# Optimization experiments

Measured on AMD Instinct MI355X. Metric: run time of the kernel, lower is better.

The kernel has to match this reference:

```python
import jax, jax.numpy as jnp
import numpy as np

B = 65536
N_PTS = 11        # n_trajectory_points
N_NEWTON = 5      # shooting_max_iter (fixed-count Newton shooting)
METRIC_FLOOR = 0.1


def _metric(c, lam, W1, b1, W2, b2, W3, b3):
    # g(c, lambda) > 0 ; c, lam: [B]
    x = jnp.stack([c, lam], axis=-1)              # [B, 2]
    h = jnp.tanh(x @ W1 + b1)
    h = jnp.tanh(h @ W2 + b2)
    return jax.nn.softplus((h @ W3 + b3)[..., 0]) + METRIC_FLOOR


def _christoffel(c, lam, mp):
    # 1-D manifold: Gamma = 0.5 * (dg/dc) / g  (dg/dc via forward-mode jvp)
    g, dg = jax.jvp(lambda cc: _metric(cc, lam, *mp), (c,), (jnp.ones_like(c),))
    return 0.5 * dg / g


def _integrate(c0, v0, lam, mp, n_pts):
    # RK4 integration of geodesic ODE  c' = v, v' = -Gamma(c) v^2  on t in [0,1]
    dt = 1.0 / (n_pts - 1)

    def deriv(c, v):
        return v, -_christoffel(c, lam, mp) * v * v

    def step(carry, _):
        c, v = carry
        k1c, k1v = deriv(c, v)
        k2c, k2v = deriv(c + 0.5 * dt * k1c, v + 0.5 * dt * k1v)
        k3c, k3v = deriv(c + 0.5 * dt * k2c, v + 0.5 * dt * k2v)
        k4c, k4v = deriv(c + dt * k3c, v + dt * k3v)
        cn = c + (dt / 6.0) * (k1c + 2 * k2c + 2 * k3c + k4c)
        vn = v + (dt / 6.0) * (k1v + 2 * k2v + 2 * k3v + k4v)
        return (cn, vn), (cn, vn)

    (cf, vf), (cs, vs) = jax.lax.scan(step, (c0, v0), None, length=n_pts - 1)
    cs = jnp.concatenate([c0[None], cs], axis=0)   # [T, B]
    vs = jnp.concatenate([v0[None], vs], axis=0)   # [T, B]
    traj = jnp.stack([cs, vs], axis=-1)            # [T, B, 2]
    return cf, jnp.transpose(traj, (1, 0, 2))      # final c [B], traj [B, T, 2]


def _shoot(c0, c1, lam, mp, n_pts):
    # Batched Newton shooting on initial velocity so that c(1) == c1.
    def final_c(v0):
        return _integrate(c0, v0, lam, mp, n_pts)[0]

    def newton(v0, _):
        out, dr = jax.jvp(final_c, (v0,), (jnp.ones_like(v0),))
        dr_safe = jnp.where(jnp.abs(dr) < 1e-6, 1e-6, dr)
        return v0 - (out - c1) / dr_safe, None

    v0, _ = jax.lax.scan(newton, c1 - c0, None, length=N_NEWTON)
    return v0


def setup_inputs() -> dict:
    key = jax.random.key(0)
    ks = jax.random.split(key, 8)
    f32 = jnp.float32
    return {
        "c_source": jax.random.uniform(ks[0], (B,), dtype=f32),
        "c_target": jax.random.uniform(ks[1], (B,), dtype=f32),
        "wavelength": jax.random.uniform(ks[2], (B,), dtype=f32),
        "W1": jax.random.normal(ks[3], (2, 16), dtype=f32) * 0.5,
        "b1": jnp.zeros((16,), f32),
        "W2": jax.random.normal(ks[4], (16, 16), dtype=f32) * 0.25,
        "b2": jnp.zeros((16,), f32),
        "W3": jax.random.normal(ks[5], (16, 1), dtype=f32) * 0.25,
        "b3": jnp.zeros((1,), f32),
        "D1": jax.random.normal(ks[6], (6, 64), dtype=f32) * 0.4,
        "d1": jnp.zeros((64,), f32),
        "D2": jax.random.normal(ks[7], (64, 1), dtype=f32) * 0.125,
        "d2": jnp.zeros((1,), f32),
    }


def reference(c_source, c_target, wavelength,
              W1, b1, W2, b2, W3, b3, D1, d1, D2, d2):
    mp = (W1, b1, W2, b2, W3, b3)
    # Vectorized geodesic BVP for the whole batch (replaces the Python loop)
    v0 = _shoot(c_source, c_target, wavelength, mp, N_PTS)
    _, traj = _integrate(c_source, v0, wavelength, mp, N_PTS)  # [B, T, 2]

    # AbsorbanceDecoder: path statistics + wavelength -> MLP -> absorbance
    c = traj[..., 0]
    v = traj[..., 1]
    path_len = jnp.sum(jnp.abs(jnp.diff(c, axis=1)), axis=1)
    feats = jnp.stack([c.mean(axis=1), c[:, -1], path_len,
                       v.mean(axis=1), jnp.abs(v).max(axis=1),
                       wavelength], axis=-1)                   # [B, 6]
    h = jnp.tanh(feats @ D1 + d1)
    absorbance = (h @ D2 + d2)[..., 0]                         # [B]
    return absorbance
```

## Files before the change

kernel.cpp:

```cpp
#include <hip/hip_runtime.h>
#include <math.h>

#define NPTS 11
#define METRIC_FLOOR 0.1f

#define RAWN 32
#define RAW2 1024
#define NG 30
#define SCALE_G 27.0f
#define INV_SCALE (1.0f / 27.0f)

#define WS_S  0
#define WS_SP 1024
#define WS_H4 2048

typedef float v2f __attribute__((ext_vector_type(2)));

#define L2E 1.44269504088896340736f
#define LN2 0.69314718055994530942f

struct MW {
    float w1c[16], w1l[16], b1v[16], b2v[16], w3v[16];
};

static __device__ __forceinline__ float fast_tanh(float x) {
    float e = __builtin_amdgcn_exp2f(x * (2.0f * L2E));
    return fmaf(-2.0f, __builtin_amdgcn_rcpf(e + 1.0f), 1.0f);
}

extern "C" __global__ void table_raw_kernel(
    const float* __restrict__ W1, const float* __restrict__ b1,
    const float* __restrict__ W2, const float* __restrict__ b2,
    const float* __restrict__ W3, const float* __restrict__ b3,
    float* __restrict__ ws)
{
    __shared__ __align__(16) float sW2[256];
    const int t = threadIdx.x;
    sW2[t] = W2[t];
    __syncthreads();

    const int p = blockIdx.x * 256 + t;
    if (p >= RAW2) return;

    MW mw;
#pragma unroll
    for (int j = 0; j < 16; ++j) {
        mw.w1c[j] = W1[j];
        mw.w1l[j] = W1[16 + j];
        mw.b1v[j] = b1[j];
        mw.b2v[j] = b2[j];
        mw.w3v[j] = W3[j];
    }
    const float b3v = b3[0];

    const int ri = p & (RAWN - 1), rj = p >> 5;
    const float c   = (float)(ri - 2) * INV_SCALE;
    const float lam = (float)(rj - 2) * INV_SCALE;

    float h1[16], p1[16];
#pragma unroll
    for (int k = 0; k < 16; ++k) {
        float a  = mw.w1c[k];
        float u  = fmaf(c, a, fmaf(lam, mw.w1l[k], mw.b1v[k]));
        float t0 = fast_tanh(u);
        float s  = fmaf(-t0, t0, 1.0f);
        h1[k] = t0;
        p1[k] = s * a;
    }
    v2f U[8], DU[8];
#pragma unroll
    for (int jp = 0; jp < 8; ++jp) {
        U[jp]  = (v2f){mw.b2v[2*jp], mw.b2v[2*jp+1]};
        DU[jp] = (v2f){0.0f, 0.0f};
    }
#pragma unroll 2
    for (int i2 = 0; i2 < 16; ++i2) {
        const float4* wrow4 = reinterpret_cast<const float4*>(sW2 + i2 * 16);
        v2f hh = (v2f){h1[i2], h1[i2]};
        v2f pp = (v2f){p1[i2], p1[i2]};
#pragma unroll
        for (int q4 = 0; q4 < 4; ++q4) {
            float4 w4 = wrow4[q4];
            v2f wa = (v2f){w4.x, w4.y};
            v2f wb = (v2f){w4.z, w4.w};
            int jp = 2 * q4;
            U[jp]    = __builtin_elementwise_fma(wa, hh, U[jp]);
            DU[jp]   = __builtin_elementwise_fma(wa, pp, DU[jp]);
            U[jp+1]  = __builtin_elementwise_fma(wb, hh, U[jp+1]);
            DU[jp+1] = __builtin_elementwise_fma(wb, pp, DU[jp+1]);
        }
    }
    float z = b3v, dz = 0.0f;
#pragma unroll
    for (int jp = 0; jp < 8; ++jp)
#pragma unroll
        for (int k = 0; k < 2; ++k) {
            float u  = U[jp][k];
            float du = DU[jp][k];
            float t0 = fast_tanh(u);
            float s  = fmaf(-t0, t0, 1.0f);
            float w3 = mw.w3v[2*jp+k];
            z  = fmaf(t0, w3, z);
            dz = fmaf(s * du, w3, dz);
        }
    float az  = fabsf(z);
    float em  = __builtin_amdgcn_exp2f(-az * L2E);
    float r1  = __builtin_amdgcn_rcpf(1.0f + em);
    float spv = fmaxf(z, 0.0f) + __builtin_amdgcn_logf(1.0f + em) * LN2;
    float sig = (z >= 0.0f) ? r1 : (1.0f - r1);
    float g   = spv + METRIC_FLOOR;
    float dg  = sig * dz;

    float s  = sqrtf(g);
    ws[WS_S  + p] = s;
    ws[WS_SP + p] = 0.5f * dg * __builtin_amdgcn_rcpf(s);
}

extern "C" __global__ __launch_bounds__(1024)
void table_build_kernel(float* __restrict__ ws)
{
    __shared__ float lF[RAW2];
    __shared__ float ls[RAW2];

    const int t = threadIdx.x;
    const int i = t & (RAWN - 1);

    float s  = ws[WS_S + t];
    float sp = ws[WS_SP + t];
    float s_prev  = __shfl_up(s, 1, 32);
    float sp_prev = __shfl_up(sp, 1, 32);

    const float h  = INV_SCALE;
    const float h2 = h * h * (1.0f / 12.0f);
    float inc = (i == 0) ? 0.0f
              : 0.5f * h * (s_prev + s) + h2 * (sp_prev - sp);

    float F = inc;
#pragma unroll
    for (int d = 1; d < 32; d <<= 1) {
        float o = __shfl_up(F, (unsigned)d, 32);
        if (i >= d) F += o;
    }

    lF[t] = F;
    ls[t] = s;
    __syncthreads();

    if (t < NG * NG) {
        const int ii = t % NG, jj = t / NG;
        const int ri = ii + 1, rj = jj + 1;
        float Fv = lF[rj * RAWN + ri];
        float sv = ls[rj * RAWN + ri];
        float FY = 0.5f * (lF[(rj + 1) * RAWN + ri] - lF[(rj - 1) * RAWN + ri]);
        float sY = 0.5f * (ls[(rj + 1) * RAWN + ri] - ls[(rj - 1) * RAWN + ri]);
        reinterpret_cast<float4*>(ws + WS_H4)[t] = make_float4(Fv, sv, FY, sY);
    }
}

static __device__ __forceinline__ void feval(
    const float4* __restrict__ r0, const float4* __restrict__ r1,
    float hy0, float hy1, float hy2, float hy3, float X,
    float& F_out, float& d_out)
{
    float fx = floorf(X);
    fx = fminf(fmaxf(fx, 0.0f), (float)(NG - 2));
    float tx = X - fx;
    int i0 = (int)fx;
    float t2 = tx * tx, t3 = t2 * tx;
    float h00 = fmaf(2.0f, t3, fmaf(-3.0f, t2, 1.0f));
    float h10 = t3 - 2.0f * t2 + tx;
    float h01 = fmaf(-2.0f, t3, 3.0f * t2);
    float h11 = t3 - t2;
    float d00 = 6.0f * (t2 - tx);
    float d10 = fmaf(3.0f, t2, fmaf(-4.0f, tx, 1.0f));
    float d01 = -d00;
    float d11 = fmaf(3.0f, t2, -2.0f * tx);

    float4 a0 = r0[i0], b0 = r0[i0 + 1];
    float4 a1 = r1[i0], b1 = r1[i0 + 1];
    const float h = INV_SCALE;

    float Fc0  = fmaf(h00, a0.x, fmaf(h10, h * a0.y, fmaf(h01, b0.x, h11 * (h * b0.y))));
    float dF0  = fmaf(d00, a0.x, fmaf(d10, h * a0.y, fmaf(d01, b0.x, d11 * (h * b0.y))));
    float FY0  = fmaf(h00, a0.z, fmaf(h10, h * a0.w, fmaf(h01, b0.z, h11 * (h * b0.w))));
    float dFY0 = fmaf(d00, a0.z, fmaf(d10, h * a0.w, fmaf(d01, b0.z, d11 * (h * b0.w))));
    float Fc1  = fmaf(h00, a1.x, fmaf(h10, h * a1.y, fmaf(h01, b1.x, h11 * (h * b1.y))));
    float dF1  = fmaf(d00, a1.x, fmaf(d10, h * a1.y, fmaf(d01, b1.x, d11 * (h * b1.y))));
    float FY1  = fmaf(h00, a1.z, fmaf(h10, h * a1.w, fmaf(h01, b1.z, h11 * (h * b1.w))));
    float dFY1 = fmaf(d00, a1.z, fmaf(d10, h * a1.w, fmaf(d01, b1.z, d11 * (h * b1.w))));

    F_out = fmaf(hy0, Fc0, fmaf(hy1, FY0, fmaf(hy2, Fc1, hy3 * FY1)));
    d_out = fmaf(hy0, dF0, fmaf(hy1, dFY0, fmaf(hy2, dF1, hy3 * dFY1)));
}

extern "C" __global__ __launch_bounds__(256, 1)
void geodesic_kernel(const float* __restrict__ gc0, const float* __restrict__ gc1,
                     const float* __restrict__ glam,
                     const float* __restrict__ D1, const float* __restrict__ d1,
                     const float* __restrict__ D2, const float* __restrict__ d2,
                     const float* __restrict__ ws,
                     float* __restrict__ out, int n)
{
    __shared__ __align__(16) float4 sH[NG * NG];
    __shared__ __align__(16) float  sD1[6 * 64];
    __shared__ __align__(16) float  sd1[64];
    __shared__ __align__(16) float  sD2[64];

    const int t = threadIdx.x;

    {
        const float4* wsH4 = reinterpret_cast<const float4*>(ws + WS_H4);
        const float4* D1f  = reinterpret_cast<const float4*>(D1);
        const float4* d1f  = reinterpret_cast<const float4*>(d1);
        const float4* D2f  = reinterpret_cast<const float4*>(D2);

        float4 hbuf[3];
#pragma unroll
        for (int k = 0; k < 3; ++k) hbuf[k] = wsH4[k * 256 + t];
        float4 tail_h = make_float4(0.f, 0.f, 0.f, 0.f);
        float4 tail_d = tail_h;
        if (t < 132) tail_h = wsH4[768 + t];
        if (t < 128) tail_d = (t < 96) ? D1f[t]
                             : (t < 112 ? d1f[t - 96] : D2f[t - 112]);

        float4* sD1f = reinterpret_cast<float4*>(sD1);
        float4* sd1f = reinterpret_cast<float4*>(sd1);
        float4* sD2f = reinterpret_cast<float4*>(sD2);
#pragma unroll
        for (int k = 0; k < 3; ++k) sH[k * 256 + t] = hbuf[k];
        if (t < 132) sH[768 + t] = tail_h;
        if (t < 128) {
            if (t < 96)       sD1f[t]       = tail_d;
            else if (t < 112) sd1f[t - 96]  = tail_d;
            else              sD2f[t - 112] = tail_d;
        }
    }
    __syncthreads();

    const int idx = blockIdx.x * blockDim.x + t;
    if (idx >= n) return;

    const float d2v = d2[0];
    const float c0  = gc0[idx];
    const float c1  = gc1[idx];
    const float lam = glam[idx];

    float sy = fmaf(lam, SCALE_G, 1.0f);
    float fy = fminf(fmaxf(floorf(sy), 0.0f), (float)(NG - 2));
    float ty = sy - fy;
    int j0 = (int)fy;
    float ty2 = ty * ty, ty3 = ty2 * ty;
    const float hy0 = fmaf(2.0f, ty3, fmaf(-3.0f, ty2, 1.0f));
    const float hy1 = ty3 - 2.0f * ty2 + ty;
    const float hy2 = fmaf(-2.0f, ty3, 3.0f * ty2);
    const float hy3 = ty3 - ty2;
    const float4* gr0 = sH + j0 * NG;
    const float4* gr1 = gr0 + NG;

    const float X0 = fmaf(c0, SCALE_G, 1.0f);
    const float X1 = fmaf(c1, SCALE_G, 1.0f);
    float F0, dd0, F1, dd1;
    feval(gr0, gr1, hy0, hy1, hy2, hy3, X0, F0, dd0);
    feval(gr0, gr1, hy0, hy1, hy2, hy3, X1, F1, dd1);
    const float L = F1 - F0;

    float X[9], dlast[9];
#pragma unroll
    for (int i = 0; i < 9; ++i)
        X[i] = fmaf((float)(i + 1) * 0.1f, X1 - X0, X0);
#pragma unroll
    for (int it = 0; it < 3; ++it) {
#pragma unroll
        for (int i = 0; i < 9; ++i) {
            float F, d;
            feval(gr0, gr1, hy0, hy1, hy2, hy3, X[i], F, d);
            float Ti = fmaf((float)(i + 1) * 0.1f, L, F0);
            X[i] -= (F - Ti) * __builtin_amdgcn_rcpf(d);
            dlast[i] = d;
        }
    }

    const float Lh = L * INV_SCALE;
    float csum = c0 + c1;
    float r0e = __builtin_amdgcn_rcpf(dd0);
    float r1e = __builtin_amdgcn_rcpf(dd1);
    float rsum = r0e + r1e;
    float rmax = fmaxf(r0e, r1e);
#pragma unroll
    for (int i = 0; i < 9; ++i) {
        csum += (X[i] - 1.0f) * INV_SCALE;
        float r = __builtin_amdgcn_rcpf(dlast[i]);
        rsum += r;
        rmax = fmaxf(rmax, r);
    }
    const float vsum = Lh * rsum;
    const float vmax = fabsf(Lh) * rmax;
    const float plen = fabsf(c1 - c0);

    const float inv_npts = 1.0f / (float)NPTS;
    const float f0 = csum * inv_npts;
    const float f1 = c1;
    const float f2 = plen;
    const float f3 = vsum * inv_npts;
    const float f4 = vmax;
    const float f5 = lam;

    float acc = d2v;
#pragma unroll 4
    for (int j = 0; j < 64; ++j) {
        float u = sd1[j];
        u = fmaf(f0, sD1[0 * 64 + j], u);
        u = fmaf(f1, sD1[1 * 64 + j], u);
        u = fmaf(f2, sD1[2 * 64 + j], u);
        u = fmaf(f3, sD1[3 * 64 + j], u);
        u = fmaf(f4, sD1[4 * 64 + j], u);
        u = fmaf(f5, sD1[5 * 64 + j], u);
        acc = fmaf(fast_tanh(u), sD2[j], acc);
    }
    out[idx] = acc;
}

extern "C" void kernel_launch(void* const* d_in, const int* in_sizes, int n_in,
                              void* d_out, int out_size, void* d_ws, size_t ws_size,
                              hipStream_t stream) {
    const float* c_source   = (const float*)d_in[0];
    const float* c_target   = (const float*)d_in[1];
    const float* wavelength = (const float*)d_in[2];
    const float* W1 = (const float*)d_in[3];
    const float* b1 = (const float*)d_in[4];
    const float* W2 = (const float*)d_in[5];
    const float* b2 = (const float*)d_in[6];
    const float* W3 = (const float*)d_in[7];
    const float* b3 = (const float*)d_in[8];
    const float* D1 = (const float*)d_in[9];
    const float* d1 = (const float*)d_in[10];
    const float* D2 = (const float*)d_in[11];
    const float* d2 = (const float*)d_in[12];
    float* out = (float*)d_out;
    float* ws  = (float*)d_ws;

    const int n = in_sizes[0];

    hipLaunchKernelGGL(table_raw_kernel, dim3(RAW2 / 256), dim3(256), 0,
                       stream, W1, b1, W2, b2, W3, b3, ws);
    hipLaunchKernelGGL(table_build_kernel, dim3(1), dim3(1024), 0, stream, ws);

    const int block = 256;
    const int grid  = (n + block - 1) / block;
    hipLaunchKernelGGL(geodesic_kernel, dim3(grid), dim3(block), 0, stream,
                       c_source, c_target, wavelength,
                       D1, d1, D2, d2, ws, out, n);
}
```

Measured before the change: 21.14 us.

## Fold table-build prefix scan into geodesic kernel prologue, drop separate launch

```diff
diff --git a/kernel.cpp b/kernel.cpp
--- a/kernel.cpp
+++ b/kernel.cpp
@@ -12,7 +12,6 @@
 
 #define WS_S  0
 #define WS_SP 1024
-#define WS_H4 2048
 
 typedef float v2f __attribute__((ext_vector_type(2)));
 
@@ -114,47 +113,6 @@
     float s  = sqrtf(g);
     ws[WS_S  + p] = s;
     ws[WS_SP + p] = 0.5f * dg * __builtin_amdgcn_rcpf(s);
-}
-
-extern "C" __global__ __launch_bounds__(1024)
-void table_build_kernel(float* __restrict__ ws)
-{
-    __shared__ float lF[RAW2];
-    __shared__ float ls[RAW2];
-
-    const int t = threadIdx.x;
-    const int i = t & (RAWN - 1);
-
-    float s  = ws[WS_S + t];
-    float sp = ws[WS_SP + t];
-    float s_prev  = __shfl_up(s, 1, 32);
-    float sp_prev = __shfl_up(sp, 1, 32);
-
-    const float h  = INV_SCALE;
-    const float h2 = h * h * (1.0f / 12.0f);
-    float inc = (i == 0) ? 0.0f
-              : 0.5f * h * (s_prev + s) + h2 * (sp_prev - sp);
-
-    float F = inc;
-#pragma unroll
-    for (int d = 1; d < 32; d <<= 1) {
-        float o = __shfl_up(F, (unsigned)d, 32);
-        if (i >= d) F += o;
-    }
-
-    lF[t] = F;
-    ls[t] = s;
-    __syncthreads();
-
-    if (t < NG * NG) {
-        const int ii = t % NG, jj = t / NG;
-        const int ri = ii + 1, rj = jj + 1;
-        float Fv = lF[rj * RAWN + ri];
-        float sv = ls[rj * RAWN + ri];
-        float FY = 0.5f * (lF[(rj + 1) * RAWN + ri] - lF[(rj - 1) * RAWN + ri]);
-        float sY = 0.5f * (ls[(rj + 1) * RAWN + ri] - ls[(rj - 1) * RAWN + ri]);
-        reinterpret_cast<float4*>(ws + WS_H4)[t] = make_float4(Fv, sv, FY, sY);
-    }
 }
 
 static __device__ __forceinline__ void feval(
@@ -201,6 +159,9 @@
                      const float* __restrict__ ws,
                      float* __restrict__ out, int n)
 {
+    __shared__ __align__(16) float  ls[RAW2];
+    __shared__ __align__(16) float  lsp[RAW2];
+    __shared__ __align__(16) float  lF[RAW2];
     __shared__ __align__(16) float4 sH[NG * NG];
     __shared__ __align__(16) float  sD1[6 * 64];
     __shared__ __align__(16) float  sd1[64];
@@ -209,31 +170,59 @@
     const int t = threadIdx.x;
 
     {
-        const float4* wsH4 = reinterpret_cast<const float4*>(ws + WS_H4);
-        const float4* D1f  = reinterpret_cast<const float4*>(D1);
-        const float4* d1f  = reinterpret_cast<const float4*>(d1);
-        const float4* D2f  = reinterpret_cast<const float4*>(D2);
-
-        float4 hbuf[3];
-#pragma unroll
-        for (int k = 0; k < 3; ++k) hbuf[k] = wsH4[k * 256 + t];
-        float4 tail_h = make_float4(0.f, 0.f, 0.f, 0.f);
-        float4 tail_d = tail_h;
-        if (t < 132) tail_h = wsH4[768 + t];
+        const float4* wsS4  = reinterpret_cast<const float4*>(ws + WS_S);
+        const float4* wsSP4 = reinterpret_cast<const float4*>(ws + WS_SP);
+        const float4* D1f   = reinterpret_cast<const float4*>(D1);
+        const float4* d1f   = reinterpret_cast<const float4*>(d1);
+        const float4* D2f   = reinterpret_cast<const float4*>(D2);
+
+        float4 sv  = wsS4[t];
+        float4 spv = wsSP4[t];
+        float4 tail_d = make_float4(0.f, 0.f, 0.f, 0.f);
         if (t < 128) tail_d = (t < 96) ? D1f[t]
                              : (t < 112 ? d1f[t - 96] : D2f[t - 112]);
 
-        float4* sD1f = reinterpret_cast<float4*>(sD1);
-        float4* sd1f = reinterpret_cast<float4*>(sd1);
-        float4* sD2f = reinterpret_cast<float4*>(sD2);
-#pragma unroll
-        for (int k = 0; k < 3; ++k) sH[k * 256 + t] = hbuf[k];
-        if (t < 132) sH[768 + t] = tail_h;
+        reinterpret_cast<float4*>(ls)[t]  = sv;
+        reinterpret_cast<float4*>(lsp)[t] = spv;
         if (t < 128) {
-            if (t < 96)       sD1f[t]       = tail_d;
-            else if (t < 112) sd1f[t - 96]  = tail_d;
-            else              sD2f[t - 112] = tail_d;
-        }
+            if (t < 96)       reinterpret_cast<float4*>(sD1)[t]       = tail_d;
+            else if (t < 112) reinterpret_cast<float4*>(sd1)[t - 96]  = tail_d;
+            else              reinterpret_cast<float4*>(sD2)[t - 112] = tail_d;
+        }
+    }
+    __syncthreads();
+
+    {
+        const float h  = INV_SCALE;
+        const float h2 = h * h * (1.0f / 12.0f);
+#pragma unroll
+        for (int k = 0; k < 4; ++k) {
+            const int p = t + k * 256;
+            const int col = p & (RAWN - 1);
+            float s  = ls[p];
+            float sp = lsp[p];
+            float s_prev  = __shfl_up(s, 1, 32);
+            float sp_prev = __shfl_up(sp, 1, 32);
+            float F = (col == 0) ? 0.0f
+                    : 0.5f * h * (s_prev + s) + h2 * (sp_prev - sp);
+#pragma unroll
+            for (int d = 1; d < 32; d <<= 1) {
+                float o = __shfl_up(F, (unsigned)d, 32);
+                if (col >= d) F += o;
+            }
+            lF[p] = F;
+        }
+    }
+    __syncthreads();
+
+    for (int p = t; p < NG * NG; p += 256) {
+        const int ii = p % NG, jj = p / NG;
+        const int ri = ii + 1, rj = jj + 1;
+        float Fv = lF[rj * RAWN + ri];
+        float sv = ls[rj * RAWN + ri];
+        float FY = 0.5f * (lF[(rj + 1) * RAWN + ri] - lF[(rj - 1) * RAWN + ri]);
+        float sY = 0.5f * (ls[(rj + 1) * RAWN + ri] - ls[(rj - 1) * RAWN + ri]);
+        sH[p] = make_float4(Fv, sv, FY, sY);
     }
     __syncthreads();
 
@@ -343,7 +332,6 @@
 
     hipLaunchKernelGGL(table_raw_kernel, dim3(RAW2 / 256), dim3(256), 0,
                        stream, W1, b1, W2, b2, W3, b3, ws);
-    hipLaunchKernelGGL(table_build_kernel, dim3(1), dim3(1024), 0, stream, ws);
 
     const int block = 256;
     const int grid  = (n + block - 1) / block;
```

New measurement: 19.57 us, median of 2. 1.08x faster.
